# Performance work log

Hardware: AMD Instinct MI355X
Metric: run time of the kernel (lower is better)

Reference implementation:

```python
import math
import jax, jax.numpy as jnp
import numpy as np

D_MODEL = 1024
NUM_HEADS = 16
HEAD_DIM = D_MODEL // NUM_HEADS
B, T = 4, 2048


def _get_slopes(n_heads: int) -> np.ndarray:
    def pow2_slopes(n):
        start = 2 ** (-(2 ** (-(math.log2(n) - 3))))
        return [start * start ** i for i in range(n)]
    if math.log2(n_heads).is_integer():
        return np.array(pow2_slopes(n_heads), dtype=np.float32)
    closest = 2 ** math.floor(math.log2(n_heads))
    slopes = pow2_slopes(closest)
    slopes += pow2_slopes(2 * closest)[0::2][: n_heads - closest]
    return np.array(slopes[:n_heads], dtype=np.float32)


def setup_inputs() -> dict:
    key = jax.random.key(0)
    ks = jax.random.split(key, 6)
    init = 0.02
    return {
        "x": jax.random.normal(ks[0], (B, T, D_MODEL), dtype=jnp.float32),
        "wq": jax.random.normal(ks[1], (D_MODEL, D_MODEL), dtype=jnp.float32) * init,
        "wk": jax.random.normal(ks[2], (D_MODEL, D_MODEL), dtype=jnp.float32) * init,
        "wv": jax.random.normal(ks[3], (D_MODEL, D_MODEL), dtype=jnp.float32) * init,
        "wo": jax.random.normal(ks[4], (D_MODEL, D_MODEL), dtype=jnp.float32) * init,
        "bo": jnp.zeros((D_MODEL,), dtype=jnp.float32),
    }


def reference(x, wq, wk, wv, wo, bo):
    Bx, Tx, _ = x.shape
    H, Dh = NUM_HEADS, HEAD_DIM
    scale = math.sqrt(Dh)
    # nn.Linear: y = x @ W^T
    q = (x @ wq.T).reshape(Bx, Tx, H, Dh).transpose(0, 2, 1, 3)  # (B,H,T,D)
    k = (x @ wk.T).reshape(Bx, Tx, H, Dh).transpose(0, 2, 1, 3)
    v = (x @ wv.T).reshape(Bx, Tx, H, Dh).transpose(0, 2, 1, 3)
    attn = jnp.einsum("bhqd,bhkd->bhqk", q, k) / scale
    # ALiBi bias: -slope * |i - j|, symmetric distance as in the source
    pos = jnp.arange(Tx)
    dist = -jnp.abs(pos[None, :] - pos[:, None]).astype(jnp.float32)  # (T,T)
    slopes = jnp.asarray(_get_slopes(H))  # (H,)
    attn = attn + slopes[None, :, None, None] * dist[None, None, :, :]
    attn = jax.nn.softmax(attn, axis=-1)
    out = jnp.einsum("bhqk,bhkd->bhqd", attn, v)
    out = out.transpose(0, 2, 1, 3).reshape(Bx, Tx, H * Dh)
    return out @ wo.T + bo
```

## Files before the change

kernel.cpp:

```cpp
#include <hip/hip_runtime.h>

#define DMODEL 1024
#define NHEADS 16
#define HDIM   64
#define BB     4
#define TT     2048

typedef __attribute__((ext_vector_type(8))) short bf16x8;
typedef __attribute__((ext_vector_type(4))) short bf16x4;
typedef __attribute__((ext_vector_type(4))) float f32x4;

#if __has_builtin(__builtin_amdgcn_exp2f)
#define EXP2(x) __builtin_amdgcn_exp2f(x)
#else
#define EXP2(x) __expf(0.69314718f * (x))
#endif

#define C1SCALE 0.18033688f

__device__ inline void async16(const void* g, void* l) {
  __builtin_amdgcn_global_load_lds(
      (const __attribute__((address_space(1))) unsigned int*)g,
      (__attribute__((address_space(3))) unsigned int*)l,
      16, 0, 0);
}

__device__ inline unsigned short f2bf(float x) {
  union { float f; unsigned int u; } c; c.f = x;
  unsigned int r = (c.u + 0x7FFFu + ((c.u >> 16) & 1u)) >> 16;
  return (unsigned short)r;
}

__device__ inline unsigned int pkbf(float x, float y) {
  union { float f; unsigned int u; } a, b; a.f = x; b.f = y;
  return __builtin_amdgcn_perm(b.u, a.u, 0x07060302u);
}

__global__ __launch_bounds__(256) void cvt_all(
    const float* __restrict__ x,  const float* __restrict__ wq,
    const float* __restrict__ wk, const float* __restrict__ wv,
    const float* __restrict__ wo,
    unsigned short* __restrict__ xb, unsigned short* __restrict__ wqkvb,
    unsigned short* __restrict__ wob)
{
  int bid = blockIdx.x;
  const float* src; unsigned short* dst; size_t off;
  if (bid < 8192) { src = x; dst = xb; off = (size_t)bid * 1024; }
  else {
    int w = (bid - 8192) >> 10, r = (bid - 8192) & 1023;
    off = (size_t)r * 1024;
    if (w == 0)      { src = wq; dst = wqkvb; }
    else if (w == 1) { src = wk; dst = wqkvb + 1048576; }
    else if (w == 2) { src = wv; dst = wqkvb + 2097152; }
    else             { src = wo; dst = wob; }
  }
  size_t i = off + threadIdx.x * 4;
  float4 v = *(const float4*)(src + i);
  ushort4 o;
  o.x = f2bf(v.x); o.y = f2bf(v.y); o.z = f2bf(v.z); o.w = f2bf(v.w);
  *(ushort4*)(dst + i) = o;
}

__global__ __launch_bounds__(512, 4) void gemm_qkv(
    const unsigned short* __restrict__ A, const unsigned short* __restrict__ W,
    unsigned short* __restrict__ qw, unsigned short* __restrict__ kw,
    unsigned short* __restrict__ vtw)
{
  __shared__ unsigned short As[2][128 * 64];
  __shared__ unsigned short Bs[2][128 * 64];
  const int tid  = threadIdx.x;
  const int lane = tid & 63;
  const int wave = tid >> 6;
  const int lo   = lane & 15, q4 = lane >> 4;
  const int lo7  = lane & 7;
  const int wm   = wave & 3, wn = wave >> 2;
  const int m0 = blockIdx.x * 128;
  const int nb = blockIdx.y;
  const int n0 = nb * 128;
  const int mid = nb >> 3;

  f32x4 acc[2][4] = {};

  auto stage = [&](int k0, int buf) {
#pragma unroll
    for (int i = 0; i < 2; ++i) {
      int ci = i * 512 + tid;
      int row = ci >> 3;
      int c = (ci & 7) ^ (row & 7);
      async16(A + (size_t)(m0 + row) * DMODEL + k0 + c * 8, (char*)As[buf] + ci * 16);
      async16(W + (size_t)(n0 + row) * DMODEL + k0 + c * 8, (char*)Bs[buf] + ci * 16);
    }
  };

  stage(0, 0);
  for (int it = 0; it < DMODEL / 64; ++it) {
    const int buf = it & 1;
    __syncthreads();
    if (it + 1 < DMODEL / 64) stage((it + 1) * 64, buf ^ 1);
#pragma unroll
    for (int hh = 0; hh < 2; ++hh) {
      bf16x8 af[2], bf[4];
#pragma unroll
      for (int mi = 0; mi < 2; ++mi)
        af[mi] = *(const bf16x8*)&As[buf][(wm * 32 + mi * 16 + lo) * 64 + ((hh * 4 + q4) ^ lo7) * 8];
#pragma unroll
      for (int ni = 0; ni < 4; ++ni)
        bf[ni] = *(const bf16x8*)&Bs[buf][(wn * 64 + ni * 16 + lo) * 64 + ((hh * 4 + q4) ^ lo7) * 8];
#pragma unroll
      for (int mi = 0; mi < 2; ++mi)
#pragma unroll
        for (int ni = 0; ni < 4; ++ni)
          acc[mi][ni] = __builtin_amdgcn_mfma_f32_16x16x32_bf16(af[mi], bf[ni], acc[mi][ni], 0, 0, 0);
    }
  }

  unsigned short* dst = (mid == 0) ? qw : (mid == 1) ? kw : vtw;
  const float sc = (mid == 0) ? C1SCALE : 1.0f;
#pragma unroll
  for (int mi = 0; mi < 2; ++mi) {
#pragma unroll
    for (int ni = 0; ni < 4; ++ni) {
#pragma unroll
      for (int r = 0; r < 4; ++r) {
        int m = m0 + wm * 32 + mi * 16 + q4 * 4 + r;
        int nl = ((nb & 7) * 128) + wn * 64 + ni * 16 + lo;
        float v = acc[mi][ni][r] * sc;
        int b = m >> 11, t = m & (TT - 1);
        int h = nl >> 6, d = nl & 63;
        if (mid == 2)
          dst[(((size_t)(b * NHEADS + h)) * HDIM + d) * TT + t] = f2bf(v);
        else
          dst[(((size_t)(b * NHEADS + h)) * TT + t) * HDIM + d] = f2bf(v);
      }
    }
  }
}

__global__ __launch_bounds__(512, 4) void gemm_out(
    const unsigned short* __restrict__ A, const unsigned short* __restrict__ W,
    const float* __restrict__ bias, float* __restrict__ C)
{
  __shared__ unsigned short As[2][128 * 64];
  __shared__ unsigned short Bs[2][128 * 64];
  const int tid  = threadIdx.x;
  const int lane = tid & 63;
  const int wave = tid >> 6;
  const int lo   = lane & 15, q4 = lane >> 4;
  const int lo7  = lane & 7;
  const int wm   = wave & 3, wn = wave >> 2;
  const int m0 = blockIdx.x * 128, n0 = blockIdx.y * 128;

  f32x4 acc[2][4] = {};

  auto stage = [&](int k0, int buf) {
#pragma unroll
    for (int i = 0; i < 2; ++i) {
      int ci = i * 512 + tid;
      int row = ci >> 3;
      int c = (ci & 7) ^ (row & 7);
      async16(A + (size_t)(m0 + row) * DMODEL + k0 + c * 8, (char*)As[buf] + ci * 16);
      async16(W + (size_t)(n0 + row) * DMODEL + k0 + c * 8, (char*)Bs[buf] + ci * 16);
    }
  };

  stage(0, 0);
  for (int it = 0; it < DMODEL / 64; ++it) {
    const int buf = it & 1;
    __syncthreads();
    if (it + 1 < DMODEL / 64) stage((it + 1) * 64, buf ^ 1);
#pragma unroll
    for (int hh = 0; hh < 2; ++hh) {
      bf16x8 af[2], bf[4];
#pragma unroll
      for (int mi = 0; mi < 2; ++mi)
        af[mi] = *(const bf16x8*)&As[buf][(wm * 32 + mi * 16 + lo) * 64 + ((hh * 4 + q4) ^ lo7) * 8];
#pragma unroll
      for (int ni = 0; ni < 4; ++ni)
        bf[ni] = *(const bf16x8*)&Bs[buf][(wn * 64 + ni * 16 + lo) * 64 + ((hh * 4 + q4) ^ lo7) * 8];
#pragma unroll
      for (int mi = 0; mi < 2; ++mi)
#pragma unroll
        for (int ni = 0; ni < 4; ++ni)
          acc[mi][ni] = __builtin_amdgcn_mfma_f32_16x16x32_bf16(af[mi], bf[ni], acc[mi][ni], 0, 0, 0);
    }
  }

#pragma unroll
  for (int mi = 0; mi < 2; ++mi)
#pragma unroll
    for (int ni = 0; ni < 4; ++ni)
#pragma unroll
      for (int r = 0; r < 4; ++r) {
        int m = m0 + wm * 32 + mi * 16 + q4 * 4 + r;
        int n = n0 + wn * 64 + ni * 16 + lo;
        C[(size_t)m * DMODEL + n] = acc[mi][ni][r] + bias[n];
      }
}

__global__ __launch_bounds__(512, 4) void attn_kernel(
    const unsigned short* __restrict__ Q, const unsigned short* __restrict__ K,
    const unsigned short* __restrict__ Vt, unsigned short* __restrict__ O)
{
  __shared__ unsigned short Ks[2][64 * 64];
  __shared__ unsigned short Vs[2][64 * 64];

  const int tid = threadIdx.x, lane = tid & 63, wave = tid >> 6;
  const int lo = lane & 15, q4 = lane >> 4;
  const int lo7 = lane & 7;
  const int bid = blockIdx.x;
  const int h  = (int)((0x3201765489ABFEDCull >> ((bid >> 5) * 4)) & 15);
  const int qb = bid & 7;
  const int b  = (bid >> 3) & 3;
  const int bh = b * NHEADS + h;
  const float slopeL = exp2f(-0.5f * (float)(h + 1)) * 1.44269504f;
  const int q0 = qb * 256;
  const int wq0 = q0 + wave * 32;

  const int D = (int)(19.407f * exp2f(0.5f * (float)(h + 1)));
  int tlo = q0 - D;
  const int ktlo = (tlo <= 0) ? 0 : (tlo >> 6);
  int thi = (q0 + 255 + D) >> 6;
  const int kthi = (thi > TT / 64 - 1) ? TT / 64 - 1 : thi;

  bf16x8 qf[2][2];
#pragma unroll
  for (int m = 0; m < 2; ++m)
#pragma unroll
    for (int hh = 0; hh < 2; ++hh)
      qf[m][hh] = *(const bf16x8*)(Q + ((size_t)bh * TT + wq0 + m * 16 + lo) * HDIM + hh * 32 + q4 * 8);

  bf16x8 ones8;
  {
    short o = (lo == 0) ? (short)0x3F80 : (short)0;
    ones8 = bf16x8{o, o, o, o, o, o, o, o};
  }

  f32x4 Oacc[2][4];
  f32x4 lacc[2];
#pragma unroll
  for (int m = 0; m < 2; ++m) {
    lacc[m] = f32x4{0.f, 0.f, 0.f, 0.f};
#pragma unroll
    for (int nd = 0; nd < 4; ++nd) Oacc[m][nd] = f32x4{0.f, 0.f, 0.f, 0.f};
  }

  float eb[2][4];
#pragma unroll
  for (int m = 0; m < 2; ++m)
#pragma unroll
    for (int r = 0; r < 4; ++r)
      eb[m][r] = (float)(wq0 + m * 16 + lo - q4 * 4 - r);

  const unsigned short* kbh = K + (size_t)bh * TT * HDIM;
  const unsigned short* vbh = Vt + (size_t)bh * HDIM * TT;

  auto stage = [&](int kt, int buf) {
    int ci = tid;
    int row = ci >> 3;
    int c = (ci & 7) ^ (row & 7);
    async16(kbh + (size_t)(kt * 64 + row) * HDIM + c * 8, (char*)Ks[buf] + ci * 16);
    async16(vbh + (size_t)row * TT + kt * 64 + c * 8,     (char*)Vs[buf] + ci * 16);
  };

  stage(ktlo, 0);

  for (int kt = ktlo; kt <= kthi; ++kt) {
    const int buf = (kt - ktlo) & 1;
    __syncthreads();
    if (kt < kthi) stage(kt + 1, buf ^ 1);

#pragma unroll
    for (int pp = 0; pp < 2; ++pp) {
      unsigned int ua[2][2], ub[2][2];
#pragma unroll
      for (int hns = 0; hns < 2; ++hns) {
        const int ns = pp * 2 + hns;
        const int krow = (ns * 16 + lo) * 64;
        bf16x8 kf0 = *(const bf16x8*)&Ks[buf][krow + ((q4) ^ lo7) * 8];
        bf16x8 kf1 = *(const bf16x8*)&Ks[buf][krow + ((4 + q4) ^ lo7) * 8];
        const float kb = (float)(kt * 64 + ns * 16);
#pragma unroll
        for (int m = 0; m < 2; ++m) {
          f32x4 a = {0.f, 0.f, 0.f, 0.f};
          __builtin_amdgcn_s_setprio(1);
          a = __builtin_amdgcn_mfma_f32_16x16x32_bf16(kf0, qf[m][0], a, 0, 0, 0);
          a = __builtin_amdgcn_mfma_f32_16x16x32_bf16(kf1, qf[m][1], a, 0, 0, 0);
          __builtin_amdgcn_s_setprio(0);
          float pv[4];
#pragma unroll
          for (int r = 0; r < 4; ++r) {
            float w = eb[m][r] - kb;
            pv[r] = EXP2(fmaf(-slopeL, fabsf(w), a[r]));
          }
          ua[hns][m] = pkbf(pv[0], pv[1]);
          ub[hns][m] = pkbf(pv[2], pv[3]);
        }
      }

      bf16x8 paf[2];
#pragma unroll
      for (int m = 0; m < 2; ++m) {
        unsigned int w0 = ua[0][m], w2 = ua[1][m];
        unsigned int w1 = ub[0][m], w3 = ub[1][m];
        asm("v_permlane32_swap_b32 %0, %1" : "+v"(w0), "+v"(w2));
        asm("v_permlane16_swap_b32 %0, %1" : "+v"(w0), "+v"(w2));
        asm("v_permlane32_swap_b32 %0, %1" : "+v"(w1), "+v"(w3));
        asm("v_permlane16_swap_b32 %0, %1" : "+v"(w1), "+v"(w3));
        union { bf16x8 v; unsigned int u[4]; } U;
        U.u[0] = w0; U.u[1] = w1; U.u[2] = w2; U.u[3] = w3;
        paf[m] = U.v;
      }

#pragma unroll
      for (int nd = 0; nd < 4; ++nd) {
        const int row = nd * 16 + lo;
        bf16x8 vb = *(const bf16x8*)&Vs[buf][row * 64 + ((pp * 4 + q4) ^ lo7) * 8];
        __builtin_amdgcn_s_setprio(1);
#pragma unroll
        for (int m = 0; m < 2; ++m)
          Oacc[m][nd] = __builtin_amdgcn_mfma_f32_16x16x32_bf16(paf[m], vb, Oacc[m][nd], 0, 0, 0);
        __builtin_amdgcn_s_setprio(0);
      }
#pragma unroll
      for (int m = 0; m < 2; ++m)
        lacc[m] = __builtin_amdgcn_mfma_f32_16x16x32_bf16(paf[m], ones8, lacc[m], 0, 0, 0);
    }
  }

#pragma unroll
  for (int m = 0; m < 2; ++m)
#pragma unroll
    for (int r = 0; r < 4; ++r) {
      float l = __shfl(lacc[m][r], lane & 48);
      float inv = 1.f / l;
      int t = wq0 + m * 16 + q4 * 4 + r;
#pragma unroll
      for (int nd = 0; nd < 4; ++nd) {
        int d = nd * 16 + lo;
        O[((size_t)(b * TT + t)) * DMODEL + h * HDIM + d] = f2bf(Oacc[m][nd][r] * inv);
      }
    }
}

extern "C" void kernel_launch(void* const* d_in, const int* in_sizes, int n_in,
                              void* d_out, int out_size, void* d_ws, size_t ws_size,
                              hipStream_t stream) {
  const float* x  = (const float*)d_in[0];
  const float* wq = (const float*)d_in[1];
  const float* wk = (const float*)d_in[2];
  const float* wv = (const float*)d_in[3];
  const float* wo = (const float*)d_in[4];
  const float* bo = (const float*)d_in[5];
  float* out = (float*)d_out;

  char* ws = (char*)d_ws;
  const size_t seg  = (size_t)BB * TT * DMODEL * sizeof(unsigned short);
  const size_t wseg = (size_t)DMODEL * DMODEL * sizeof(unsigned short);
  unsigned short* qw    = (unsigned short*)(ws);
  unsigned short* kw    = (unsigned short*)(ws + seg);
  unsigned short* vtw   = (unsigned short*)(ws + 2 * seg);
  unsigned short* ow    = (unsigned short*)(ws + 3 * seg);
  unsigned short* xb    = (unsigned short*)(ws + 4 * seg);
  unsigned short* wqkvb = (unsigned short*)(ws + 5 * seg);
  unsigned short* wob   = (unsigned short*)(ws + 5 * seg + 3 * wseg);

  cvt_all<<<dim3(8192 + 4096), dim3(256), 0, stream>>>(x, wq, wk, wv, wo, xb, wqkvb, wob);

  gemm_qkv<<<dim3(64, 24), dim3(512), 0, stream>>>(xb, wqkvb, qw, kw, vtw);

  attn_kernel<<<dim3(BB * NHEADS * (TT / 256)), dim3(512), 0, stream>>>(qw, kw, vtw, ow);

  gemm_out<<<dim3(64, 8), dim3(512), 0, stream>>>(ow, wob, bo, out);
}
```

Baseline: 244.0 us.

## Replace MFMA row-sum with VALU sums, RNE bf16 pack, vector V stores, reorder blocks

```diff
diff --git a/kernel.cpp b/kernel.cpp
--- a/kernel.cpp
+++ b/kernel.cpp
@@ -31,9 +31,10 @@
   return (unsigned short)r;
 }
 
-__device__ inline unsigned int pkbf(float x, float y) {
-  union { float f; unsigned int u; } a, b; a.f = x; b.f = y;
-  return __builtin_amdgcn_perm(b.u, a.u, 0x07060302u);
+__device__ inline unsigned int pkbf_rne(float x, float y) {
+  unsigned int r;
+  asm("v_cvt_pk_bf16_f32 %0, %1, %2" : "=v"(r) : "v"(x), "v"(y));
+  return r;
 }
 
 __global__ __launch_bounds__(256) void cvt_all(
@@ -120,17 +121,23 @@
   for (int mi = 0; mi < 2; ++mi) {
 #pragma unroll
     for (int ni = 0; ni < 4; ++ni) {
-#pragma unroll
-      for (int r = 0; r < 4; ++r) {
-        int m = m0 + wm * 32 + mi * 16 + q4 * 4 + r;
-        int nl = ((nb & 7) * 128) + wn * 64 + ni * 16 + lo;
-        float v = acc[mi][ni][r] * sc;
-        int b = m >> 11, t = m & (TT - 1);
-        int h = nl >> 6, d = nl & 63;
-        if (mid == 2)
-          dst[(((size_t)(b * NHEADS + h)) * HDIM + d) * TT + t] = f2bf(v);
-        else
-          dst[(((size_t)(b * NHEADS + h)) * TT + t) * HDIM + d] = f2bf(v);
+      int m_ = m0 + wm * 32 + mi * 16 + q4 * 4;
+      int nl = ((nb & 7) * 128) + wn * 64 + ni * 16 + lo;
+      int b_ = m_ >> 11, t_ = m_ & (TT - 1);
+      int h_ = nl >> 6, d_ = nl & 63;
+      if (mid == 2) {
+        ushort4 o4;
+        o4.x = f2bf(acc[mi][ni][0]);
+        o4.y = f2bf(acc[mi][ni][1]);
+        o4.z = f2bf(acc[mi][ni][2]);
+        o4.w = f2bf(acc[mi][ni][3]);
+        *(ushort4*)&dst[(((size_t)(b_ * NHEADS + h_)) * HDIM + d_) * TT + t_] = o4;
+      } else {
+#pragma unroll
+        for (int r = 0; r < 4; ++r) {
+          float v = acc[mi][ni][r] * sc;
+          dst[(((size_t)(b_ * NHEADS + h_)) * TT + t_ + r) * HDIM + d_] = f2bf(v);
+        }
       }
     }
   }
@@ -208,9 +215,11 @@
   const int lo = lane & 15, q4 = lane >> 4;
   const int lo7 = lane & 7;
   const int bid = blockIdx.x;
-  const int h  = (int)((0x3201765489ABFEDCull >> ((bid >> 5) * 4)) & 15);
-  const int qb = bid & 7;
-  const int b  = (bid >> 3) & 3;
+  const int g   = (bid & 7) + 8 * (bid >> 6);
+  const int qb  = (bid >> 3) & 7;
+  const int slot = g >> 2;
+  const int b   = g & 3;
+  const int h  = (int)((0x3201765489ABFEDCull >> (slot * 4)) & 15);
   const int bh = b * NHEADS + h;
   const float slopeL = exp2f(-0.5f * (float)(h + 1)) * 1.44269504f;
   const int q0 = qb * 256;
@@ -229,20 +238,12 @@
     for (int hh = 0; hh < 2; ++hh)
       qf[m][hh] = *(const bf16x8*)(Q + ((size_t)bh * TT + wq0 + m * 16 + lo) * HDIM + hh * 32 + q4 * 8);
 
-  bf16x8 ones8;
-  {
-    short o = (lo == 0) ? (short)0x3F80 : (short)0;
-    ones8 = bf16x8{o, o, o, o, o, o, o, o};
-  }
-
   f32x4 Oacc[2][4];
-  f32x4 lacc[2];
-#pragma unroll
-  for (int m = 0; m < 2; ++m) {
-    lacc[m] = f32x4{0.f, 0.f, 0.f, 0.f};
+  float ps[2] = {0.f, 0.f};
+#pragma unroll
+  for (int m = 0; m < 2; ++m)
 #pragma unroll
     for (int nd = 0; nd < 4; ++nd) Oacc[m][nd] = f32x4{0.f, 0.f, 0.f, 0.f};
-  }
 
   float eb[2][4];
 #pragma unroll
@@ -292,8 +293,9 @@
             float w = eb[m][r] - kb;
             pv[r] = EXP2(fmaf(-slopeL, fabsf(w), a[r]));
           }
-          ua[hns][m] = pkbf(pv[0], pv[1]);
-          ub[hns][m] = pkbf(pv[2], pv[3]);
+          ps[m] += (pv[0] + pv[1]) + (pv[2] + pv[3]);
+          ua[hns][m] = pkbf_rne(pv[0], pv[1]);
+          ub[hns][m] = pkbf_rne(pv[2], pv[3]);
         }
       }
 
@@ -321,17 +323,20 @@
           Oacc[m][nd] = __builtin_amdgcn_mfma_f32_16x16x32_bf16(paf[m], vb, Oacc[m][nd], 0, 0, 0);
         __builtin_amdgcn_s_setprio(0);
       }
-#pragma unroll
-      for (int m = 0; m < 2; ++m)
-        lacc[m] = __builtin_amdgcn_mfma_f32_16x16x32_bf16(paf[m], ones8, lacc[m], 0, 0, 0);
-    }
+    }
+  }
+
+#pragma unroll
+  for (int m = 0; m < 2; ++m) {
+    ps[m] += __shfl_xor(ps[m], 16);
+    ps[m] += __shfl_xor(ps[m], 32);
   }
 
 #pragma unroll
   for (int m = 0; m < 2; ++m)
 #pragma unroll
     for (int r = 0; r < 4; ++r) {
-      float l = __shfl(lacc[m][r], lane & 48);
+      float l = __shfl(ps[m], q4 * 4 + r);
       float inv = 1.f / l;
       int t = wq0 + m * 16 + q4 * 4 + r;
 #pragma unroll
```

After: 233.9 us. -4.1%, faster.
